# Kernel optimization log

Measured on AMD Instinct MI355X. Metric: run time of the kernel, lower is better.

Reference implementation:

```python
import jax, jax.numpy as jnp
import numpy as np

N_NODES = 100000
N_EDGES = 3200000
PERIODS = 12
C_IN, C_OUT, F_OUT = 1, 4, 12


def setup_inputs() -> dict:
    key = jax.random.key(0)
    ks = jax.random.split(key, 20)
    s = 0.1
    return {
        "x": jax.random.normal(ks[0], (N_NODES, C_IN, PERIODS), dtype=jnp.float32),
        "edge_index": jax.random.randint(ks[1], (2, N_EDGES), 0, N_NODES, dtype=jnp.int32),
        "conv_z_w": s * jax.random.normal(ks[2], (C_IN, C_OUT), dtype=jnp.float32),
        "conv_z_b": s * jax.random.normal(ks[3], (C_OUT,), dtype=jnp.float32),
        "lin_z_w": s * jax.random.normal(ks[4], (2 * C_OUT, C_OUT), dtype=jnp.float32),
        "lin_z_b": s * jax.random.normal(ks[5], (C_OUT,), dtype=jnp.float32),
        "conv_r_w": s * jax.random.normal(ks[6], (C_IN, C_OUT), dtype=jnp.float32),
        "conv_r_b": s * jax.random.normal(ks[7], (C_OUT,), dtype=jnp.float32),
        "lin_r_w": s * jax.random.normal(ks[8], (2 * C_OUT, C_OUT), dtype=jnp.float32),
        "lin_r_b": s * jax.random.normal(ks[9], (C_OUT,), dtype=jnp.float32),
        "conv_h_w": s * jax.random.normal(ks[10], (C_IN, C_OUT), dtype=jnp.float32),
        "conv_h_b": s * jax.random.normal(ks[11], (C_OUT,), dtype=jnp.float32),
        "lin_h_w": s * jax.random.normal(ks[12], (2 * C_OUT, C_OUT), dtype=jnp.float32),
        "lin_h_b": s * jax.random.normal(ks[13], (C_OUT,), dtype=jnp.float32),
        "att": jax.random.normal(ks[14], (PERIODS,), dtype=jnp.float32),
        "out_w": s * jax.random.normal(ks[15], (C_OUT, F_OUT), dtype=jnp.float32),
        "out_b": s * jax.random.normal(ks[16], (F_OUT,), dtype=jnp.float32),
        "f": 12,
    }


def reference(x, edge_index, conv_z_w, conv_z_b, lin_z_w, lin_z_b,
              conv_r_w, conv_r_b, lin_r_w, lin_r_b,
              conv_h_w, conv_h_b, lin_h_w, lin_h_b,
              att, out_w, out_b, f):
    N, _, P = x.shape
    loops = jnp.arange(N, dtype=edge_index.dtype)
    src = jnp.concatenate([edge_index[0], loops])  # self loops, fill=1
    dst = jnp.concatenate([edge_index[1], loops])
    deg = jax.ops.segment_sum(jnp.ones_like(src, dtype=x.dtype), dst, num_segments=N)
    dinv = jnp.where(deg > 0, jax.lax.rsqrt(deg), 0.0)
    norm = dinv[src] * dinv[dst]  # [E+N] symmetric GCN normalization

    def gcn(xt, W, b):
        xw = xt @ W  # [N, C_OUT]
        msg = xw[src] * norm[:, None]
        return jax.ops.segment_sum(msg, dst, num_segments=N) + b

    H0 = jnp.zeros((N, conv_z_w.shape[1]), dtype=x.dtype)

    def tgcn_step(xt):  # xt: [N, C_IN]; A3TGCN does not carry H across periods
        z = jax.nn.sigmoid(jnp.concatenate([gcn(xt, conv_z_w, conv_z_b), H0], 1) @ lin_z_w + lin_z_b)
        r = jax.nn.sigmoid(jnp.concatenate([gcn(xt, conv_r_w, conv_r_b), H0], 1) @ lin_r_w + lin_r_b)
        h_t = jnp.tanh(jnp.concatenate([gcn(xt, conv_h_w, conv_h_b), r * H0], 1) @ lin_h_w + lin_h_b)
        return z * H0 + (1.0 - z) * h_t

    xs = jnp.transpose(x, (2, 0, 1))  # [P, N, C_IN]
    Hs = jax.vmap(tgcn_step)(xs)  # [P, N, C_OUT]
    probs = jax.nn.softmax(att)
    H_accum = jnp.einsum('p,pnd->nd', probs, Hs)  # attention over periods
    out = H_accum @ out_w + out_b  # [N, 12]
    return out[:, :f]
```

## Files before the change

kernel.cpp:

```cpp
#include <hip/hip_runtime.h>
#include <hip/hip_fp16.h>
#include <math.h>


#define PERIODS 12
#define BSZ     256
#define BSH     8
#define STRIDE  9216
#define SRCBITS 17
#define SMASK   ((1 << SRCBITS) - 1)
#define CH      4096

struct Consts {
    float az[4], cz[4], ah[4], ch[4], probs[PERIODS];
};

typedef float vf2 __attribute__((ext_vector_type(2)));

__device__ __forceinline__ float dec1_manual(unsigned b) {
    unsigned e = (b >> 3) & 15u, m = b & 7u;
    float v = e ? __uint_as_float(((e + 120u) << 23) | (m << 20))
                : (float)m * 0.001953125f;
    return (b & 0x80u) ? -v : v;
}

__device__ __forceinline__ void dec4(unsigned u, float* o) {
#if __has_builtin(__builtin_amdgcn_cvt_pk_f32_fp8)
    vf2 lo = __builtin_amdgcn_cvt_pk_f32_fp8((int)u, false);
    vf2 hi = __builtin_amdgcn_cvt_pk_f32_fp8((int)u, true);
    o[0] = lo.x; o[1] = lo.y; o[2] = hi.x; o[3] = hi.y;
#else
    o[0] = dec1_manual(u & 255u);
    o[1] = dec1_manual((u >> 8) & 255u);
    o[2] = dec1_manual((u >> 16) & 255u);
    o[3] = dec1_manual(u >> 24);
#endif
}

__device__ __forceinline__ unsigned enc1_manual(float x) {
    unsigned s = (__float_as_uint(x) >> 24) & 0x80u;
    float a = fabsf(x);
    if (!(a > 0.f)) return s;
    a = fminf(a, 448.f);
    int eb = (int)(__float_as_uint(a) >> 23) - 127;
    int e = eb < -6 ? -6 : eb;
    float q = rintf(a * exp2f((float)(3 - e)));
    if (q >= 16.f) { e++; q = rintf(a * exp2f((float)(3 - e))); }
    if (e > 8) return s | 0x7Eu;
    int m = (int)q;
    unsigned ee, mm;
    if (m >= 8) { ee = (unsigned)(e + 7); mm = (unsigned)(m - 8); }
    else        { ee = 0u; mm = (unsigned)m; }
    return s | (ee << 3) | mm;
}

__device__ __forceinline__ unsigned pk4(float a, float b, float c, float d) {
#if __has_builtin(__builtin_amdgcn_cvt_pk_fp8_f32)
    int v = __builtin_amdgcn_cvt_pk_fp8_f32(a, b, 0, false);
    v = __builtin_amdgcn_cvt_pk_fp8_f32(c, d, v, true);
    return (unsigned)v;
#else
    return enc1_manual(a) | (enc1_manual(b) << 8) |
           (enc1_manual(c) << 16) | (enc1_manual(d) << 24);
#endif
}


__global__ __launch_bounds__(512) void k_setup(const float* conv_z_w, const float* conv_z_b,
                        const float* lin_z_w, const float* lin_z_b,
                        const float* conv_h_w, const float* conv_h_b,
                        const float* lin_h_w, const float* lin_h_b,
                        const float* att, Consts* C, int* gcur, int NB)
{
    int t = threadIdx.x;
    for (int i = t; i < NB; i += 512) gcur[i] = 0;
    if (t == 0) {
        for (int c = 0; c < 4; ++c) {
            float az = 0.f, cz = 0.f, ah = 0.f, ch = 0.f;
            for (int k = 0; k < 4; ++k) {
                az += conv_z_w[k] * lin_z_w[k * 4 + c];
                cz += conv_z_b[k] * lin_z_w[k * 4 + c];
                ah += conv_h_w[k] * lin_h_w[k * 4 + c];
                ch += conv_h_b[k] * lin_h_w[k * 4 + c];
            }
            C->az[c] = az; C->cz[c] = cz + lin_z_b[c];
            C->ah[c] = ah; C->ch[c] = ch + lin_h_b[c];
        }
        float m = att[0];
        for (int p = 1; p < PERIODS; ++p) m = fmaxf(m, att[p]);
        float e[PERIODS]; float s = 0.f;
        for (int p = 0; p < PERIODS; ++p) { e[p] = expf(att[p] - m); s += e[p]; }
        for (int p = 0; p < PERIODS; ++p) C->probs[p] = e[p] / s;
    }
}

__global__ __launch_bounds__(512) void k_binA(const int* __restrict__ ei,
                                              int* __restrict__ gcur,
                                              int* __restrict__ binned, int E) {
    __shared__ int hist[512];
    __shared__ int scn[512];
    __shared__ int gdel[512];
    __shared__ int sv[CH];
    __shared__ int sa[CH];
    int t = threadIdx.x;
    hist[t] = 0;
    __syncthreads();
    int base = blockIdx.x * CH;
    int lim = min(E - base, CH);
    #pragma unroll
    for (int k = 0; k < CH / 512; ++k) {
        int i = t + k * 512;
        if (i < lim) atomicAdd(&hist[ei[E + base + i] >> BSH], 1);
    }
    __syncthreads();
    int v = hist[t];
    scn[t] = v;
    __syncthreads();
    for (int off = 1; off < 512; off <<= 1) {
        int tmp = (t >= off) ? scn[t - off] : 0;
        __syncthreads();
        scn[t] += tmp;
        __syncthreads();
    }
    int excl = scn[t] - v;
    int g = (v > 0) ? atomicAdd(&gcur[t], v) : 0;
    gdel[t] = t * STRIDE + g - excl;
    hist[t] = excl;
    __syncthreads();
    #pragma unroll
    for (int k = 0; k < CH / 512; ++k) {
        int i = t + k * 512;
        if (i < lim) {
            int s = ei[base + i];
            int d = ei[E + base + i];
            int b = d >> BSH;
            int pos = atomicAdd(&hist[b], 1);
            sv[pos] = ((d & (BSZ - 1)) << SRCBITS) | s;
            sa[pos] = gdel[b] + pos;
        }
    }
    __syncthreads();
    for (int j = t; j < lim; j += 512)
        binned[sa[j]] = sv[j];
}

__global__ __launch_bounds__(512) void k_binB(const int* __restrict__ binned,
                                              const int* __restrict__ gcur,
                                              int* __restrict__ nodesorted,
                                              int* __restrict__ nofs) {
    __shared__ int hist[BSZ];
    __shared__ int scn[512];
    __shared__ int cur[BSZ];
    __shared__ int sorted[STRIDE];
    int b = blockIdx.x, t = threadIdx.x;
    if (t < BSZ) hist[t] = 0;
    __syncthreads();
    int cnt = gcur[b];
    const int* bb = binned + b * STRIDE;
    for (int i = t; i < cnt; i += 512)
        atomicAdd(&hist[bb[i] >> SRCBITS], 1);
    __syncthreads();
    int v = (t < BSZ) ? hist[t] : 0;
    scn[t] = v;
    __syncthreads();
    for (int off = 1; off < 512; off <<= 1) {
        int tmp = (t >= off) ? scn[t - off] : 0;
        __syncthreads();
        scn[t] += tmp;
        __syncthreads();
    }
    if (t < BSZ) {
        int excl = scn[t] - v;
        cur[t] = excl;
        nofs[b * BSZ + t] = excl;
    }
    __syncthreads();
    for (int i = t; i < cnt; i += 512) {
        int pv = bb[i];
        int pos = atomicAdd(&cur[pv >> SRCBITS], 1);
        sorted[pos] = pv & SMASK;
    }
    __syncthreads();
    int* dst = nodesorted + b * STRIDE;
    for (int j = t; j < cnt; j += 512)
        dst[j] = sorted[j];
}

__global__ void k_prep(const int* __restrict__ nofs, const int* __restrict__ gcur,
                       const float* __restrict__ x, float* __restrict__ dinv,
                       uint4* __restrict__ xs8, int N) {
    int n = blockIdx.x * blockDim.x + threadIdx.x;
    if (n >= N) return;
    int b = n >> BSH, ln = n & (BSZ - 1);
    int start = nofs[b * BSZ + ln];
    int end = (ln == BSZ - 1) ? gcur[b] : nofs[b * BSZ + ln + 1];
    float di = rsqrtf((float)(end - start) + 1.0f);
    dinv[n] = di;
    const float4* xv = (const float4*)(x + (size_t)n * PERIODS);
    float4 v0 = xv[0], v1 = xv[1], v2 = xv[2];
    uint4 r;
    r.x = pk4(v0.x * di, v0.y * di, v0.z * di, v0.w * di);
    r.y = pk4(v1.x * di, v1.y * di, v1.z * di, v1.w * di);
    r.z = pk4(v2.x * di, v2.y * di, v2.z * di, v2.w * di);
    r.w = 0;
    xs8[n] = r;
}

__device__ __forceinline__ void accdec(float* acc, uint4 r) {
    float f[PERIODS];
    dec4(r.x, f + 0); dec4(r.y, f + 4); dec4(r.z, f + 8);
    #pragma unroll
    for (int k = 0; k < PERIODS; ++k) acc[k] += f[k];
}

__global__ __launch_bounds__(512) void k_aggF(const int* __restrict__ nodesorted,
                                              const int* __restrict__ nofs,
                                              const int* __restrict__ gcur,
                                              const float* __restrict__ dinv,
                                              const uint4* __restrict__ xs8,
                                              const Consts* __restrict__ C,
                                              const float* __restrict__ out_w,
                                              const float* __restrict__ out_b,
                                              float* __restrict__ out, int N) {
    int t = threadIdx.x;
    int b = blockIdx.x >> 1;
    int half = blockIdx.x & 1;
    int ln = half * 128 + (t >> 2);
    int lane = t & 3;
    int n = (b << BSH) + ln;

    int start = nofs[b * BSZ + ln];
    int end = (ln == BSZ - 1) ? gcur[b] : nofs[b * BSZ + ln + 1];
    const int* ns = nodesorted + b * STRIDE;

    float acc[PERIODS];
    #pragma unroll
    for (int k = 0; k < PERIODS; ++k) acc[k] = 0.f;

    int i = start + lane;
    for (; i + 12 < end; i += 16) {
        int s0 = ns[i];
        int s1 = ns[i + 4];
        int s2 = ns[i + 8];
        int s3 = ns[i + 12];
        uint4 r0 = xs8[s0];
        uint4 r1 = xs8[s1];
        uint4 r2 = xs8[s2];
        uint4 r3 = xs8[s3];
        accdec(acc, r0);
        accdec(acc, r1);
        accdec(acc, r2);
        accdec(acc, r3);
    }
    for (; i < end; i += 4) {
        uint4 r0 = xs8[ns[i]];
        accdec(acc, r0);
    }

    #pragma unroll
    for (int k = 0; k < PERIODS; ++k) {
        acc[k] += __shfl_xor(acc[k], 1);
        acc[k] += __shfl_xor(acc[k], 2);
    }

    if (lane != 0 || n >= N) return;

    {
        float f[PERIODS];
        uint4 r = xs8[n];
        dec4(r.x, f + 0); dec4(r.y, f + 4); dec4(r.z, f + 8);
        #pragma unroll
        for (int k = 0; k < PERIODS; ++k) acc[k] += f[k];
    }

    float di = dinv[n];
    float hacc[4] = {0.f, 0.f, 0.f, 0.f};
    #pragma unroll
    for (int p = 0; p < PERIODS; ++p) {
        float ap = di * acc[p];
        float pr = C->probs[p];
        #pragma unroll
        for (int c = 0; c < 4; ++c) {
            float zz = 1.f / (1.f + __expf(-(ap * C->az[c] + C->cz[c])));
            float hh = tanhf(ap * C->ah[c] + C->ch[c]);
            hacc[c] += pr * (1.f - zz) * hh;
        }
    }
    float o[PERIODS];
    #pragma unroll
    for (int f = 0; f < PERIODS; ++f) {
        float v = out_b[f];
        #pragma unroll
        for (int c = 0; c < 4; ++c) v += hacc[c] * out_w[c * PERIODS + f];
        o[f] = v;
    }
    float4* ov = (float4*)(out + (size_t)n * PERIODS);
    ov[0] = make_float4(o[0], o[1], o[2],  o[3]);
    ov[1] = make_float4(o[4], o[5], o[6],  o[7]);
    ov[2] = make_float4(o[8], o[9], o[10], o[11]);
}

extern "C" void kernel_launch(void* const* d_in, const int* in_sizes, int n_in,
                              void* d_out, int out_size, void* d_ws, size_t ws_size,
                              hipStream_t stream) {
    const float* x        = (const float*)d_in[0];
    const int*   ei       = (const int*)d_in[1];
    const float* conv_z_w = (const float*)d_in[2];
    const float* conv_z_b = (const float*)d_in[3];
    const float* lin_z_w  = (const float*)d_in[4];
    const float* lin_z_b  = (const float*)d_in[5];
    const float* conv_h_w = (const float*)d_in[10];
    const float* conv_h_b = (const float*)d_in[11];
    const float* lin_h_w  = (const float*)d_in[12];
    const float* lin_h_b  = (const float*)d_in[13];
    const float* att      = (const float*)d_in[14];
    const float* out_w    = (const float*)d_in[15];
    const float* out_b    = (const float*)d_in[16];
    float* out = (float*)d_out;

    const int N  = in_sizes[0] / PERIODS;
    const int E  = in_sizes[1] / 2;
    const int NB = (N + BSZ - 1) / BSZ;
    const int gA = (E + CH - 1) / CH;

    char* ws = (char*)d_ws;
    size_t off = 0;
    Consts* consts     = (Consts*)(ws + off);  off += (sizeof(Consts) + 255) & ~255ull;
    int*    gcur       = (int*)(ws + off);     off += ((size_t)NB * 4 + 255) & ~255ull;
    float*  dinv       = (float*)(ws + off);   off += ((size_t)N * 4 + 255) & ~255ull;
    uint4*  xs8        = (uint4*)(ws + off);   off += ((size_t)(N + 256) * 16 + 255) & ~255ull;
    int*    binned     = (int*)(ws + off);     off += ((size_t)NB * STRIDE * 4 + 255) & ~255ull;
    int*    nodesorted = (int*)(ws + off);     off += ((size_t)NB * STRIDE * 4 + 255) & ~255ull;
    int*    nofs       = (int*)(ws + off);     off += ((size_t)NB * BSZ * 4 + 255) & ~255ull;
    (void)ws_size; (void)n_in; (void)out_size;

    k_setup<<<1, 512, 0, stream>>>(conv_z_w, conv_z_b, lin_z_w, lin_z_b,
                                   conv_h_w, conv_h_b, lin_h_w, lin_h_b, att,
                                   consts, gcur, NB);
    k_binA<<<gA, 512, 0, stream>>>(ei, gcur, binned, E);
    k_binB<<<NB, 512, 0, stream>>>(binned, gcur, nodesorted, nofs);
    k_prep<<<(N + 255) / 256, 256, 0, stream>>>(nofs, gcur, x, dinv, xs8, N);
    k_aggF<<<NB * 2, 512, 0, stream>>>(nodesorted, nofs, gcur, dinv, xs8, consts,
                                       out_w, out_b, out, N);
}
```

Before: 184.8 us.

## Fuse per-destination sort into aggregation kernel, drop nodesorted global buffer

```diff
diff --git a/kernel.cpp b/kernel.cpp
--- a/kernel.cpp
+++ b/kernel.cpp
@@ -6,7 +6,9 @@
 #define PERIODS 12
 #define BSZ     256
 #define BSH     8
+#define HALF    128
 #define STRIDE  9216
+#define SCAP    4800
 #define SRCBITS 17
 #define SMASK   ((1 << SRCBITS) - 1)
 #define CH      4096
@@ -70,10 +72,12 @@
                         const float* lin_z_w, const float* lin_z_b,
                         const float* conv_h_w, const float* conv_h_b,
                         const float* lin_h_w, const float* lin_h_b,
-                        const float* att, Consts* C, int* gcur, int NB)
+                        const float* att, Consts* C, int* gcur, int NB,
+                        unsigned short* deg16, int N, int NPAD)
 {
     int t = threadIdx.x;
     for (int i = t; i < NB; i += 512) gcur[i] = 0;
+    for (int i = N + t; i < NPAD; i += 512) deg16[i] = 0;
     if (t == 0) {
         for (int c = 0; c < 4; ++c) {
             float az = 0.f, cz = 0.f, ah = 0.f, ch = 0.f;
@@ -144,66 +148,36 @@
         binned[sa[j]] = sv[j];
 }
 
-__global__ __launch_bounds__(512) void k_binB(const int* __restrict__ binned,
+__global__ __launch_bounds__(512) void k_prep(const int* __restrict__ binned,
                                               const int* __restrict__ gcur,
-                                              int* __restrict__ nodesorted,
-                                              int* __restrict__ nofs) {
-    __shared__ int hist[BSZ];
-    __shared__ int scn[512];
-    __shared__ int cur[BSZ];
-    __shared__ int sorted[STRIDE];
+                                              const float* __restrict__ x,
+                                              unsigned short* __restrict__ deg16,
+                                              uint4* __restrict__ xs8, int N) {
+    __shared__ int ldeg[BSZ];
     int b = blockIdx.x, t = threadIdx.x;
-    if (t < BSZ) hist[t] = 0;
+    if (t < BSZ) ldeg[t] = 0;
     __syncthreads();
     int cnt = gcur[b];
     const int* bb = binned + b * STRIDE;
     for (int i = t; i < cnt; i += 512)
-        atomicAdd(&hist[bb[i] >> SRCBITS], 1);
-    __syncthreads();
-    int v = (t < BSZ) ? hist[t] : 0;
-    scn[t] = v;
-    __syncthreads();
-    for (int off = 1; off < 512; off <<= 1) {
-        int tmp = (t >= off) ? scn[t - off] : 0;
-        __syncthreads();
-        scn[t] += tmp;
-        __syncthreads();
-    }
+        atomicAdd(&ldeg[bb[i] >> SRCBITS], 1);
+    __syncthreads();
     if (t < BSZ) {
-        int excl = scn[t] - v;
-        cur[t] = excl;
-        nofs[b * BSZ + t] = excl;
-    }
-    __syncthreads();
-    for (int i = t; i < cnt; i += 512) {
-        int pv = bb[i];
-        int pos = atomicAdd(&cur[pv >> SRCBITS], 1);
-        sorted[pos] = pv & SMASK;
-    }
-    __syncthreads();
-    int* dst = nodesorted + b * STRIDE;
-    for (int j = t; j < cnt; j += 512)
-        dst[j] = sorted[j];
-}
-
-__global__ void k_prep(const int* __restrict__ nofs, const int* __restrict__ gcur,
-                       const float* __restrict__ x, float* __restrict__ dinv,
-                       uint4* __restrict__ xs8, int N) {
-    int n = blockIdx.x * blockDim.x + threadIdx.x;
-    if (n >= N) return;
-    int b = n >> BSH, ln = n & (BSZ - 1);
-    int start = nofs[b * BSZ + ln];
-    int end = (ln == BSZ - 1) ? gcur[b] : nofs[b * BSZ + ln + 1];
-    float di = rsqrtf((float)(end - start) + 1.0f);
-    dinv[n] = di;
-    const float4* xv = (const float4*)(x + (size_t)n * PERIODS);
-    float4 v0 = xv[0], v1 = xv[1], v2 = xv[2];
-    uint4 r;
-    r.x = pk4(v0.x * di, v0.y * di, v0.z * di, v0.w * di);
-    r.y = pk4(v1.x * di, v1.y * di, v1.z * di, v1.w * di);
-    r.z = pk4(v2.x * di, v2.y * di, v2.z * di, v2.w * di);
-    r.w = 0;
-    xs8[n] = r;
+        int n = (b << BSH) + t;
+        if (n < N) {
+            int dg = ldeg[t];
+            deg16[n] = (unsigned short)dg;
+            float di = rsqrtf((float)dg + 1.0f);
+            const float4* xv = (const float4*)(x + (size_t)n * PERIODS);
+            float4 v0 = xv[0], v1 = xv[1], v2 = xv[2];
+            uint4 r;
+            r.x = pk4(v0.x * di, v0.y * di, v0.z * di, v0.w * di);
+            r.y = pk4(v1.x * di, v1.y * di, v1.z * di, v1.w * di);
+            r.z = pk4(v2.x * di, v2.y * di, v2.z * di, v2.w * di);
+            r.w = 0;
+            xs8[n] = r;
+        }
+    }
 }
 
 __device__ __forceinline__ void accdec(float* acc, uint4 r) {
@@ -213,47 +187,68 @@
     for (int k = 0; k < PERIODS; ++k) acc[k] += f[k];
 }
 
-__global__ __launch_bounds__(512) void k_aggF(const int* __restrict__ nodesorted,
-                                              const int* __restrict__ nofs,
-                                              const int* __restrict__ gcur,
-                                              const float* __restrict__ dinv,
-                                              const uint4* __restrict__ xs8,
-                                              const Consts* __restrict__ C,
-                                              const float* __restrict__ out_w,
-                                              const float* __restrict__ out_b,
-                                              float* __restrict__ out, int N) {
+__global__ __launch_bounds__(512) void k_agg(const int* __restrict__ binned,
+                                             const int* __restrict__ gcur,
+                                             const unsigned short* __restrict__ deg16,
+                                             const uint4* __restrict__ xs8,
+                                             const Consts* __restrict__ C,
+                                             const float* __restrict__ out_w,
+                                             const float* __restrict__ out_b,
+                                             float* __restrict__ out, int N) {
+    __shared__ int ofs[HALF + 1];
+    __shared__ int cur[HALF];
+    __shared__ int scn[HALF];
+    __shared__ int sorted[SCAP];
     int t = threadIdx.x;
     int b = blockIdx.x >> 1;
-    int half = blockIdx.x & 1;
-    int ln = half * 128 + (t >> 2);
+    int halfSel = blockIdx.x & 1;
+    int nbase = (b << BSH) + halfSel * HALF;
+
+    int d = 0;
+    if (t < HALF) { d = deg16[nbase + t]; scn[t] = d; }
+    __syncthreads();
+    for (int off = 1; off < HALF; off <<= 1) {
+        int v = (t < HALF && t >= off) ? scn[t - off] : 0;
+        __syncthreads();
+        if (t < HALF) scn[t] += v;
+        __syncthreads();
+    }
+    if (t < HALF) { int e = scn[t] - d; ofs[t] = e; cur[t] = e; }
+    if (t == HALF - 1) ofs[HALF] = scn[HALF - 1];
+    __syncthreads();
+
+    int cnt = gcur[b];
+    const int* bb = binned + b * STRIDE;
+    for (int i = t; i < cnt; i += 512) {
+        int v = bb[i];
+        int dl = v >> SRCBITS;
+        if ((dl >> 7) == halfSel) {
+            int pos = atomicAdd(&cur[dl & (HALF - 1)], 1);
+            sorted[pos] = v & SMASK;
+        }
+    }
+    __syncthreads();
+
+    int ln = t >> 2;
     int lane = t & 3;
-    int n = (b << BSH) + ln;
-
-    int start = nofs[b * BSZ + ln];
-    int end = (ln == BSZ - 1) ? gcur[b] : nofs[b * BSZ + ln + 1];
-    const int* ns = nodesorted + b * STRIDE;
+    int start = ofs[ln];
+    int end = ofs[ln + 1];
 
     float acc[PERIODS];
     #pragma unroll
     for (int k = 0; k < PERIODS; ++k) acc[k] = 0.f;
 
     int i = start + lane;
-    for (; i + 12 < end; i += 16) {
-        int s0 = ns[i];
-        int s1 = ns[i + 4];
-        int s2 = ns[i + 8];
-        int s3 = ns[i + 12];
+    for (; i + 4 < end; i += 8) {
+        int s0 = sorted[i];
+        int s1 = sorted[i + 4];
         uint4 r0 = xs8[s0];
         uint4 r1 = xs8[s1];
-        uint4 r2 = xs8[s2];
-        uint4 r3 = xs8[s3];
         accdec(acc, r0);
         accdec(acc, r1);
-        accdec(acc, r2);
-        accdec(acc, r3);
-    }
-    for (; i < end; i += 4) {
-        uint4 r0 = xs8[ns[i]];
+    }
+    if (i < end) {
+        uint4 r0 = xs8[sorted[i]];
         accdec(acc, r0);
     }
 
@@ -263,17 +258,18 @@
         acc[k] += __shfl_xor(acc[k], 2);
     }
 
-    if (lane != 0 || n >= N) return;
+    int gn = nbase + ln;
+    if (lane != 0 || gn >= N) return;
 
     {
         float f[PERIODS];
-        uint4 r = xs8[n];
+        uint4 r = xs8[gn];
         dec4(r.x, f + 0); dec4(r.y, f + 4); dec4(r.z, f + 8);
         #pragma unroll
         for (int k = 0; k < PERIODS; ++k) acc[k] += f[k];
     }
 
-    float di = dinv[n];
+    float di = rsqrtf((float)(end - start) + 1.0f);
     float hacc[4] = {0.f, 0.f, 0.f, 0.f};
     #pragma unroll
     for (int p = 0; p < PERIODS; ++p) {
@@ -294,7 +290,7 @@
         for (int c = 0; c < 4; ++c) v += hacc[c] * out_w[c * PERIODS + f];
         o[f] = v;
     }
-    float4* ov = (float4*)(out + (size_t)n * PERIODS);
+    float4* ov = (float4*)(out + (size_t)gn * PERIODS);
     ov[0] = make_float4(o[0], o[1], o[2],  o[3]);
     ov[1] = make_float4(o[4], o[5], o[6],  o[7]);
     ov[2] = make_float4(o[8], o[9], o[10], o[11]);
@@ -318,28 +314,26 @@
     const float* out_b    = (const float*)d_in[16];
     float* out = (float*)d_out;
 
-    const int N  = in_sizes[0] / PERIODS;
-    const int E  = in_sizes[1] / 2;
-    const int NB = (N + BSZ - 1) / BSZ;
-    const int gA = (E + CH - 1) / CH;
+    const int N    = in_sizes[0] / PERIODS;
+    const int E    = in_sizes[1] / 2;
+    const int NB   = (N + BSZ - 1) / BSZ;
+    const int NPAD = NB * BSZ;
+    const int gA   = (E + CH - 1) / CH;
 
     char* ws = (char*)d_ws;
     size_t off = 0;
-    Consts* consts     = (Consts*)(ws + off);  off += (sizeof(Consts) + 255) & ~255ull;
-    int*    gcur       = (int*)(ws + off);     off += ((size_t)NB * 4 + 255) & ~255ull;
-    float*  dinv       = (float*)(ws + off);   off += ((size_t)N * 4 + 255) & ~255ull;
-    uint4*  xs8        = (uint4*)(ws + off);   off += ((size_t)(N + 256) * 16 + 255) & ~255ull;
-    int*    binned     = (int*)(ws + off);     off += ((size_t)NB * STRIDE * 4 + 255) & ~255ull;
-    int*    nodesorted = (int*)(ws + off);     off += ((size_t)NB * STRIDE * 4 + 255) & ~255ull;
-    int*    nofs       = (int*)(ws + off);     off += ((size_t)NB * BSZ * 4 + 255) & ~255ull;
+    Consts*         consts = (Consts*)(ws + off);          off += (sizeof(Consts) + 255) & ~255ull;
+    int*            gcur   = (int*)(ws + off);             off += ((size_t)NB * 4 + 255) & ~255ull;
+    unsigned short* deg16  = (unsigned short*)(ws + off);  off += ((size_t)NPAD * 2 + 255) & ~255ull;
+    uint4*          xs8    = (uint4*)(ws + off);           off += ((size_t)NPAD * 16 + 255) & ~255ull;
+    int*            binned = (int*)(ws + off);             off += ((size_t)NB * STRIDE * 4 + 255) & ~255ull;
     (void)ws_size; (void)n_in; (void)out_size;
 
     k_setup<<<1, 512, 0, stream>>>(conv_z_w, conv_z_b, lin_z_w, lin_z_b,
                                    conv_h_w, conv_h_b, lin_h_w, lin_h_b, att,
-                                   consts, gcur, NB);
+                                   consts, gcur, NB, deg16, N, NPAD);
     k_binA<<<gA, 512, 0, stream>>>(ei, gcur, binned, E);
-    k_binB<<<NB, 512, 0, stream>>>(binned, gcur, nodesorted, nofs);
-    k_prep<<<(N + 255) / 256, 256, 0, stream>>>(nofs, gcur, x, dinv, xs8, N);
-    k_aggF<<<NB * 2, 512, 0, stream>>>(nodesorted, nofs, gcur, dinv, xs8, consts,
-                                       out_w, out_b, out, N);
-}
+    k_prep<<<NB, 512, 0, stream>>>(binned, gcur, x, deg16, xs8, N);
+    k_agg<<<NB * 2, 512, 0, stream>>>(binned, gcur, deg16, xs8, consts,
+                                      out_w, out_b, out, N);
+}
```

Measured after the change: 185.9 us. Within noise of the previous version (+0.6%).
